# Kernel tuning notes

Measured on AMD Instinct MI355X. Metric: run time of the kernel, lower is better.

Reference implementation:

```python
import jax, jax.numpy as jnp
import numpy as np

B, K, D, V = 8192, 32, 128, 2048
WEIGHT, SIGMA, NDCG_K = 0.15, 1.0, 10
N = K + 1


def _to_hyperboloid(x):
    # lift spatial coords onto Lorentz hyperboloid: x0 = sqrt(1 + ||x||^2)
    t = jnp.sqrt(1.0 + jnp.sum(x * x, axis=-1, keepdims=True))
    return jnp.concatenate([t, x], axis=-1)


def _lorentz_dist(u, v):
    # d(u,v) = arccosh(-<u,v>_L), <u,v>_L = -u0*v0 + u[1:].v[1:]
    inner = -u[..., 0] * v[..., 0] + jnp.sum(u[..., 1:] * v[..., 1:], axis=-1)
    return jnp.arccosh(jnp.maximum(-inner, 1.0 + 1e-7))


def setup_inputs() -> dict:
    key = jax.random.key(0)
    k = jax.random.split(key, 7)
    anchor_emb = _to_hyperboloid(jax.random.normal(k[0], (B, D), dtype=jnp.float32))
    positive_emb = _to_hyperboloid(jax.random.normal(k[1], (B, D), dtype=jnp.float32))
    negative_embs = _to_hyperboloid(jax.random.normal(k[2], (B * K, D), dtype=jnp.float32))
    tree_distances = jax.random.uniform(k[3], (V, V), dtype=jnp.float32) * 10.0
    anchor_idx = jax.random.randint(k[4], (B,), 0, V, dtype=jnp.int32)
    pos_idx = jax.random.randint(k[5], (B,), 0, V, dtype=jnp.int32)
    neg_idx = jax.random.randint(k[6], (B, K), 0, V, dtype=jnp.int32)
    return {"anchor_emb": anchor_emb, "positive_emb": positive_emb,
            "negative_embs": negative_embs, "tree_distances": tree_distances,
            "anchor_idx": anchor_idx, "pos_idx": pos_idx, "neg_idx": neg_idx}


def _lambdarank(anchor_emb, positive_emb, negative_embs, tree_distances,
                anchor_idx, pos_idx, neg_idx):
    neg = negative_embs.reshape(B, K, -1)
    pos_dist = _lorentz_dist(anchor_emb, positive_emb)            # (B,)
    neg_dists = _lorentz_dist(anchor_emb[:, None, :], neg)        # (B,K)
    d = jnp.concatenate([pos_dist[:, None], neg_dists], axis=1)   # (B,N)

    pos_t = tree_distances[anchor_idx, pos_idx]                   # (B,)
    neg_t = tree_distances[anchor_idx[:, None], neg_idx]          # (B,K)
    t = jnp.concatenate([pos_t[:, None], neg_t], axis=1)          # (B,N)
    max_t = jnp.max(t, axis=1, keepdims=True)
    rel = (max_t - t + 1e-6) / (max_t + 1e-6)                     # (B,N)

    k_top = min(NDCG_K, N)
    # 1-based rank of each item under ascending-distance sort (piecewise const)
    ranks = jnp.argsort(jnp.argsort(d, axis=1), axis=1) + 1       # (B,N)
    disc = jnp.where(ranks <= k_top,
                     1.0 / jnp.log2(ranks.astype(jnp.float32) + 1.0), 0.0)
    ideal = -jnp.sort(-rel, axis=1)[:, :k_top]                    # (B,k)
    log_pos = jnp.log2(jnp.arange(2, k_top + 2, dtype=jnp.float32))
    idcg = jnp.sum(ideal / log_pos, axis=1)                       # (B,)

    # closed-form |delta NDCG| of swapping items i,j in the ranking:
    # |(rel_i - rel_j) * (disc_i - disc_j)| / IDCG
    drel = rel[:, :, None] - rel[:, None, :]                      # (B,N,N)
    ddisc = disc[:, :, None] - disc[:, None, :]
    inv_idcg = jnp.where(idcg > 0, 1.0 / idcg, 0.0)[:, None, None]
    delta = jnp.abs(drel * ddisc) * inv_idcg

    # lambda_ij = sign(rel_i-rel_j) * delta * sigmoid(sign * sigma * (d_j - d_i))
    S = jnp.sign(drel)
    dd = d[:, None, :] - d[:, :, None]                            # d_j - d_i
    lam = S * delta * jax.nn.sigmoid(S * SIGMA * dd)
    # loss = sum_{i<j} lam_ij*(d_i-d_j); antisymmetric -> 0.5 * full sum
    loss_b = 0.5 * jnp.sum(lam * (-dd), axis=(1, 2))              # (B,)
    return WEIGHT * jnp.mean(loss_b)


def reference(anchor_emb, positive_emb, negative_embs, tree_distances,
              anchor_idx, pos_idx, neg_idx):
    return _lambdarank(anchor_emb, positive_emb, negative_embs, tree_distances,
                       anchor_idx, pos_idx, neg_idx)
```

## Files before the change

### kernel.cpp

```cpp
#include <hip/hip_runtime.h>
#include <math.h>

#define BB 8192
#define KK 32
#define DD 129
#define VV 2048
#define NN 33
#define TOPK 10
#define WPB 4

__device__ __forceinline__ float fast_rcp(float x) { return __builtin_amdgcn_rcpf(x); }
__device__ __forceinline__ float dot4(float4 a, float4 b) {
    return fmaf(a.x, b.x, fmaf(a.y, b.y, fmaf(a.z, b.z, a.w * b.w)));
}

__global__ __launch_bounds__(256) void lr_fused(
    const float* __restrict__ anchor,
    const float* __restrict__ positive,
    const float* __restrict__ neg,
    const float* __restrict__ tree,
    const int* __restrict__ a_idx,
    const int* __restrict__ p_idx,
    const int* __restrict__ n_idx,
    float* __restrict__ partial)
{
    __shared__ float  st_[WPB][NN];
    __shared__ float  sx_[WPB][NN];
    __shared__ float  sd_[WPB][NN];
    __shared__ float4 sitem[WPB][NN];

    const int t    = threadIdx.x;
    const int wave = t >> 6;
    const int lane = t & 63;
    const int g    = lane >> 4;
    const int subl = lane & 15;
    const int b    = blockIdx.x * WPB + wave;

    const int ai  = a_idx[b];
    const int col = (lane == 0) ? p_idx[b]
                                : n_idx[(size_t)b * KK + ((lane < NN ? lane : KK) - 1)];
    const float tg = tree[(size_t)ai * VV + col];
    if (lane < NN) st_[wave][lane] = tg;

    const float* ab = anchor   + (size_t)b * DD;
    const float* pb = positive + (size_t)b * DD;
    const float* nb = neg      + (size_t)b * (KK * DD);

    float4 aq0 = *(const float4*)(ab + 4 * subl);
    float4 aq1 = *(const float4*)(ab + 64 + 4 * subl);
    const float a128 = ab[128];

    const float* rp[9];
    #pragma unroll
    for (int r = 0; r < 9; ++r) {
        int row = 4 * r + g;
        if (row > KK) row = KK;
        rp[r] = (row == 0) ? pb : (nb + (size_t)(row - 1) * DD);
    }
    float4 v0[9], v1[9];
    float  t128[9];
    #pragma unroll
    for (int r = 0; r < 9; ++r) {
        v0[r]   = *(const float4*)(rp[r] + 4 * subl);
        v1[r]   = *(const float4*)(rp[r] + 64 + 4 * subl);
        t128[r] = rp[r][128];
    }

    #pragma unroll
    for (int r = 0; r < 9; ++r) {
        float s = dot4(aq0, v0[r]) + dot4(aq1, v1[r]);
        s += __shfl_xor(s, 8, 64);
        s += __shfl_xor(s, 4, 64);
        s += __shfl_xor(s, 2, 64);
        s += __shfl_xor(s, 1, 64);
        int row = 4 * r + g;
        if (subl == 0 && row < NN) {
            float full = s + a128 * t128[r];
            sx_[wave][row] = fmaxf(fmaf(2.0f * aq0.x, v0[r].x, -full), 1.0f + 1e-07f);
        }
    }

    float dlane = 0.0f;
    if (lane < NN) {
        float x = sx_[wave][lane];
        dlane = __logf(x + sqrtf(x * x - 1.0f));
        sd_[wave][lane] = dlane;
    }

    if (lane < NN) {
        float maxt = st_[wave][0];
        #pragma unroll
        for (int j = 1; j < NN; ++j) maxt = fmaxf(maxt, st_[wave][j]);
        float rel = (maxt - tg + 1e-06f) * fast_rcp(maxt + 1e-06f);

        int cnt = 0;
        #pragma unroll
        for (int j = 0; j < NN; ++j) {
            float dj = sd_[wave][j];
            cnt += (int)((dj < dlane) | ((dj == dlane) & (j < lane)));
        }
        float disc = (cnt + 1 <= TOPK) ? fast_rcp(log2f((float)(cnt + 2))) : 0.0f;
        sitem[wave][lane] = make_float4(dlane, rel, disc, 0.0f);
    }

    float c = 0.0f;
    if (lane < NN) {
        float ri = sitem[wave][lane].y;
        int pos = 0;
        #pragma unroll
        for (int j = 0; j < NN; ++j) {
            float rj = sitem[wave][j].y;
            pos += (int)((rj > ri) | ((rj == ri) & (j < lane)));
        }
        if (pos < TOPK) c = ri * fast_rcp(log2f((float)(pos + 2)));
    }
    #pragma unroll
    for (int off = 32; off > 0; off >>= 1) c += __shfl_xor(c, off, 64);
    const float inv = (c > 0.0f) ? fast_rcp(c) : 0.0f;

    float acc = 0.0f;
    #pragma unroll
    for (int it = 0; it < 9; ++it) {
        int p = it * 64 + lane;
        float vmask = (p < 528) ? 1.0f : 0.0f;
        int pc = (p < 528) ? p : 527;
        int j = (int)((1.0f + sqrtf((float)(8 * pc + 1))) * 0.5f);
        int tj = (j * (j - 1)) >> 1;
        if (tj > pc) { --j; tj = (j * (j - 1)) >> 1; }
        int i = pc - tj;
        float4 Ii = sitem[wave][i];
        float4 Ij = sitem[wave][j];
        float dd    = Ij.x - Ii.x;
        float drel  = Ii.y - Ij.y;
        float ddisc = Ii.z - Ij.z;
        float t1  = drel * fabsf(ddisc) * (inv * vmask);
        float e   = __expf(-dd);
        float num = (drel >= 0.0f) ? 1.0f : e;
        acc = fmaf(t1 * num * fast_rcp(1.0f + e), -dd, acc);
    }
    #pragma unroll
    for (int off = 32; off > 0; off >>= 1) acc += __shfl_xor(acc, off, 64);
    if (lane == 0) partial[b] = acc;
}

__global__ __launch_bounds__(256) void lr_reduce(
    const float* __restrict__ partial, float* __restrict__ out)
{
    __shared__ float swave[4];
    const float4* p4 = (const float4*)partial;
    float acc = 0.0f;
    #pragma unroll
    for (int c = 0; c < (BB / 4) / 256; ++c) {
        float4 v = p4[c * 256 + threadIdx.x];
        acc += (v.x + v.y) + (v.z + v.w);
    }
    #pragma unroll
    for (int off = 32; off > 0; off >>= 1) acc += __shfl_xor(acc, off, 64);
    if ((threadIdx.x & 63) == 0) swave[threadIdx.x >> 6] = acc;
    __syncthreads();
    if (threadIdx.x == 0)
        out[0] = (swave[0] + swave[1] + swave[2] + swave[3]) * (0.15f / (float)BB);
}

extern "C" void kernel_launch(void* const* d_in, const int* in_sizes, int n_in,
                              void* d_out, int out_size, void* d_ws, size_t ws_size,
                              hipStream_t stream)
{
    const float* anchor   = (const float*)d_in[0];
    const float* positive = (const float*)d_in[1];
    const float* neg      = (const float*)d_in[2];
    const float* tree     = (const float*)d_in[3];
    const int*   a_idx    = (const int*)d_in[4];
    const int*   p_idx    = (const int*)d_in[5];
    const int*   n_idx    = (const int*)d_in[6];
    float* partial = (float*)d_ws;

    lr_fused<<<BB / WPB, 256, 0, stream>>>(anchor, positive, neg, tree,
                                           a_idx, p_idx, n_idx, partial);
    lr_reduce<<<1, 256, 0, stream>>>(partial, (float*)d_out);
}
```

Baseline: 225.6 us.

## Fuse final reduction via atomics, chunk row loads, and merge ranking loops

Drops the separate reduction kernel: each wave atomically adds its scaled partial loss into the output, which is zeroed with an async memset before launch. Row loads are split into three chunks of three rows, cutting live registers at the cost of less memory-level parallelism. The max of tree distances now uses a wave shuffle reduction, and the ideal-ranking count is folded into the distance-rank loop by comparing tree distances directly. Per-wave float atomics make the summation order nondeterministic.

```diff
diff --git a/kernel.cpp b/kernel.cpp
--- a/kernel.cpp
+++ b/kernel.cpp
@@ -22,7 +22,7 @@
     const int* __restrict__ a_idx,
     const int* __restrict__ p_idx,
     const int* __restrict__ n_idx,
-    float* __restrict__ partial)
+    float* __restrict__ out)
 {
     __shared__ float  st_[WPB][NN];
     __shared__ float  sx_[WPB][NN];
@@ -50,33 +50,32 @@
     float4 aq1 = *(const float4*)(ab + 64 + 4 * subl);
     const float a128 = ab[128];
 
-    const float* rp[9];
     #pragma unroll
-    for (int r = 0; r < 9; ++r) {
-        int row = 4 * r + g;
-        if (row > KK) row = KK;
-        rp[r] = (row == 0) ? pb : (nb + (size_t)(row - 1) * DD);
-    }
-    float4 v0[9], v1[9];
-    float  t128[9];
-    #pragma unroll
-    for (int r = 0; r < 9; ++r) {
-        v0[r]   = *(const float4*)(rp[r] + 4 * subl);
-        v1[r]   = *(const float4*)(rp[r] + 64 + 4 * subl);
-        t128[r] = rp[r][128];
-    }
-
-    #pragma unroll
-    for (int r = 0; r < 9; ++r) {
-        float s = dot4(aq0, v0[r]) + dot4(aq1, v1[r]);
-        s += __shfl_xor(s, 8, 64);
-        s += __shfl_xor(s, 4, 64);
-        s += __shfl_xor(s, 2, 64);
-        s += __shfl_xor(s, 1, 64);
-        int row = 4 * r + g;
-        if (subl == 0 && row < NN) {
-            float full = s + a128 * t128[r];
-            sx_[wave][row] = fmaxf(fmaf(2.0f * aq0.x, v0[r].x, -full), 1.0f + 1e-07f);
+    for (int c = 0; c < 3; ++c) {
+        const float* rp[3];
+        float4 v0[3], v1[3];
+        float  t128[3];
+        #pragma unroll
+        for (int k = 0; k < 3; ++k) {
+            int row = 4 * (3 * c + k) + g;
+            if (row > KK) row = KK;
+            rp[k]   = (row == 0) ? pb : (nb + (size_t)(row - 1) * DD);
+            v0[k]   = *(const float4*)(rp[k] + 4 * subl);
+            v1[k]   = *(const float4*)(rp[k] + 64 + 4 * subl);
+            t128[k] = rp[k][128];
+        }
+        #pragma unroll
+        for (int k = 0; k < 3; ++k) {
+            float s = dot4(aq0, v0[k]) + dot4(aq1, v1[k]);
+            s += __shfl_xor(s, 8, 64);
+            s += __shfl_xor(s, 4, 64);
+            s += __shfl_xor(s, 2, 64);
+            s += __shfl_xor(s, 1, 64);
+            int row = 4 * (3 * c + k) + g;
+            if (subl == 0 && row < NN) {
+                float full = s + a128 * t128[k];
+                sx_[wave][row] = fmaxf(fmaf(2.0f * aq0.x, v0[k].x, -full), 1.0f + 1e-07f);
+            }
         }
     }
 
@@ -87,36 +86,31 @@
         sd_[wave][lane] = dlane;
     }
 
+    float tgm = (lane < NN) ? tg : -3.4e38f;
+    #pragma unroll
+    for (int off = 32; off > 0; off >>= 1)
+        tgm = fmaxf(tgm, __shfl_xor(tgm, off, 64));
+    const float maxt = tgm;
+
+    float relv = 0.0f, c0 = 0.0f;
     if (lane < NN) {
-        float maxt = st_[wave][0];
-        #pragma unroll
-        for (int j = 1; j < NN; ++j) maxt = fmaxf(maxt, st_[wave][j]);
-        float rel = (maxt - tg + 1e-06f) * fast_rcp(maxt + 1e-06f);
-
-        int cnt = 0;
+        relv = (maxt - tg + 1e-06f) * fast_rcp(maxt + 1e-06f);
+        int cnt = 0, pos = 0;
         #pragma unroll
         for (int j = 0; j < NN; ++j) {
             float dj = sd_[wave][j];
+            float tj = st_[wave][j];
             cnt += (int)((dj < dlane) | ((dj == dlane) & (j < lane)));
+            pos += (int)((tj < tg)    | ((tj == tg)    & (j < lane)));
         }
         float disc = (cnt + 1 <= TOPK) ? fast_rcp(log2f((float)(cnt + 2))) : 0.0f;
-        sitem[wave][lane] = make_float4(dlane, rel, disc, 0.0f);
+        if (pos < TOPK) c0 = relv * fast_rcp(log2f((float)(pos + 2)));
+        sitem[wave][lane] = make_float4(dlane, relv, disc, 0.0f);
     }
 
-    float c = 0.0f;
-    if (lane < NN) {
-        float ri = sitem[wave][lane].y;
-        int pos = 0;
-        #pragma unroll
-        for (int j = 0; j < NN; ++j) {
-            float rj = sitem[wave][j].y;
-            pos += (int)((rj > ri) | ((rj == ri) & (j < lane)));
-        }
-        if (pos < TOPK) c = ri * fast_rcp(log2f((float)(pos + 2)));
-    }
     #pragma unroll
-    for (int off = 32; off > 0; off >>= 1) c += __shfl_xor(c, off, 64);
-    const float inv = (c > 0.0f) ? fast_rcp(c) : 0.0f;
+    for (int off = 32; off > 0; off >>= 1) c0 += __shfl_xor(c0, off, 64);
+    const float inv = (c0 > 0.0f) ? fast_rcp(c0) : 0.0f;
 
     float acc = 0.0f;
     #pragma unroll
@@ -140,26 +134,7 @@
     }
     #pragma unroll
     for (int off = 32; off > 0; off >>= 1) acc += __shfl_xor(acc, off, 64);
-    if (lane == 0) partial[b] = acc;
-}
-
-__global__ __launch_bounds__(256) void lr_reduce(
-    const float* __restrict__ partial, float* __restrict__ out)
-{
-    __shared__ float swave[4];
-    const float4* p4 = (const float4*)partial;
-    float acc = 0.0f;
-    #pragma unroll
-    for (int c = 0; c < (BB / 4) / 256; ++c) {
-        float4 v = p4[c * 256 + threadIdx.x];
-        acc += (v.x + v.y) + (v.z + v.w);
-    }
-    #pragma unroll
-    for (int off = 32; off > 0; off >>= 1) acc += __shfl_xor(acc, off, 64);
-    if ((threadIdx.x & 63) == 0) swave[threadIdx.x >> 6] = acc;
-    __syncthreads();
-    if (threadIdx.x == 0)
-        out[0] = (swave[0] + swave[1] + swave[2] + swave[3]) * (0.15f / (float)BB);
+    if (lane == 0) atomicAdd(out, acc * (0.15f / (float)BB));
 }
 
 extern "C" void kernel_launch(void* const* d_in, const int* in_sizes, int n_in,
@@ -173,9 +148,8 @@
     const int*   a_idx    = (const int*)d_in[4];
     const int*   p_idx    = (const int*)d_in[5];
     const int*   n_idx    = (const int*)d_in[6];
-    float* partial = (float*)d_ws;
 
+    hipMemsetAsync(d_out, 0, (size_t)out_size * sizeof(float), stream);
     lr_fused<<<BB / WPB, 256, 0, stream>>>(anchor, positive, neg, tree,
-                                           a_idx, p_idx, n_idx, partial);
-    lr_reduce<<<1, 256, 0, stream>>>(partial, (float*)d_out);
+                                           a_idx, p_idx, n_idx, (float*)d_out);
 }
```

Result: slower. 295.5 us (+31.0%).
